# Kernel tuning notes

Measured on AMD Instinct MI355X. Metric: run time of the kernel, lower is better.

Reference implementation:

```python
import jax, jax.numpy as jnp
import numpy as np

NEG_INF = -1e30  # stand-in for float('-inf') that is softmax-safe


def setup_inputs() -> dict:
    key = jax.random.key(0)
    ks = jax.random.split(key, 6)
    B, H, S, D = 2, 8, 1024, 64
    NF, K = 4, 3
    return {
        "query": jax.random.normal(ks[0], (B, H, S, D), dtype=jnp.float32),
        "keys": jax.random.normal(ks[1], (B, H, S, D), dtype=jnp.float32),
        "vals": jax.random.normal(ks[2], (B, H, S, D), dtype=jnp.float32),
        "mask": jnp.ones((B, 1, S, S), dtype=jnp.int32),
        "conv_w": jax.random.normal(ks[3], (NF, 1, K, K), dtype=jnp.float32) * (1.0 / K),
        "conv_b": jnp.zeros((NF,), dtype=jnp.float32),
        "lin_w": jax.random.normal(ks[4], (1, NF), dtype=jnp.float32) * 0.5,
        "lin_b": jnp.zeros((1,), dtype=jnp.float32),
    }


def reference(query, keys, vals, mask, conv_w, conv_b, lin_w, lin_b):
    B, H, S, D = query.shape
    NF = conv_w.shape[0]
    K = conv_w.shape[2]
    scale = jnp.asarray(D, query.dtype) ** 0.5

    # [B,H,S,S] raw dot-product scores
    dp = jnp.einsum("bhsd,bhtd->bhst", query, keys) / scale

    # conv2d over the score matrix: treat (B*H) as batch, 1 input channel
    x = dp.reshape(B * H, 1, S, S)
    conv = jax.lax.conv_general_dilated(
        x, conv_w,
        window_strides=(1, 1),
        padding=[(K // 2, K // 2), (K // 2, K // 2)],
        dimension_numbers=("NCHW", "OIHW", "NCHW"),
    ) + conv_b[None, :, None, None]
    conv = jax.nn.leaky_relu(conv, negative_slope=0.01)  # [B*H, NF, S, S]

    # per-pixel linear over the filter axis (Linear(num_filters, 1))
    conv = conv.reshape(B, H, NF, S, S)
    preattn = jnp.einsum("bhfst,f->bhst", conv, lin_w[0]) + lin_b[0]

    # masking + softmax (mask broadcasts over heads)
    preattn = jnp.where(mask == 0, jnp.asarray(NEG_INF, preattn.dtype), preattn)
    attn = jax.nn.softmax(preattn, axis=-1)

    # dropout is identity in eval mode
    return jnp.einsum("bhst,bhtd->bhsd", attn, vals)
```

## Files before the change

kernel.cpp:

```cpp
#include <hip/hip_runtime.h>
#include <math.h>

#define S_LEN 1024
#define D_DIM 64
#define NBH   16
#define RPB   14
#define NSB   74

typedef unsigned short ushort_t;
typedef unsigned int uint_t;
typedef __attribute__((ext_vector_type(8))) _Float16 half8;
typedef __attribute__((ext_vector_type(2))) _Float16 h2;
typedef __attribute__((ext_vector_type(4))) short short4v;
typedef __attribute__((ext_vector_type(4))) float f32x4;

__device__ __forceinline__ ushort_t f16bits(float x) {
    _Float16 h = (_Float16)x;
    ushort_t b;
    __builtin_memcpy(&b, &h, 2);
    return b;
}
__device__ __forceinline__ float uniform_f(float x) {
    return __int_as_float(__builtin_amdgcn_readfirstlane(__float_as_int(x)));
}
__device__ __forceinline__ float fast_exp2(float x) {
#if __has_builtin(__builtin_amdgcn_exp2f)
    return __builtin_amdgcn_exp2f(x);
#else
    return exp2f(x);
#endif
}
__device__ __forceinline__ half8 mk8(uint2 a, uint2 b) {
    union { uint_t u[4]; half8 h; } c;
    c.u[0] = a.x; c.u[1] = a.y; c.u[2] = b.x; c.u[3] = b.y;
    return c.h;
}
__device__ __forceinline__ int swz(int row, int unit) {
    return (row << 4) + (((unit + (row >> 2)) & 3) << 2);
}

__global__ __launch_bounds__(256) void prep(
    const float* __restrict__ k, const float* __restrict__ v,
    const int* __restrict__ mask, const float* __restrict__ conv_w,
    ushort_t* __restrict__ kh, ushort_t* __restrict__ vh,
    unsigned* __restrict__ mw, ushort_t* __restrict__ wtab)
{
    __shared__ float Ls[64][65];
    const int tid = threadIdx.x;
    const int bx = blockIdx.x;
    if (bx < 512) {
        const int gid  = bx * 256 + tid;
        const int bh   = gid >> 13;
        const int tile = (gid >> 7) & 63;
        const int ch   = (gid >> 6) & 1;
        const int lane = gid & 63;
        const int quad = lane >> 4, t15 = lane & 15;
        const float* src = k + ((size_t)bh * S_LEN + tile * 16 + t15) * D_DIM
                             + ch * 32 + quad * 8;
        float x[8];
        *(float4*)(x + 0) = *(const float4*)(src);
        *(float4*)(x + 4) = *(const float4*)(src + 4);
        ushort_t hv[8];
        #pragma unroll
        for (int i = 0; i < 8; ++i) hv[i] = f16bits(x[i] * 0.125f);
        *(short4v*)(kh + (size_t)gid * 8)     = *(short4v*)(hv);
        *(short4v*)(kh + (size_t)gid * 8 + 4) = *(short4v*)(hv + 4);
    } else if (bx < 768) {
        const int bi = bx - 512;
        const int tt = bi & 15, bh = bi >> 4;
        const float* vb = v + ((size_t)bh * S_LEN + tt * 64) * D_DIM;
        #pragma unroll
        for (int p = 0; p < 4; ++p) {
            int idx = p * 1024 + tid * 4;
            int r = idx >> 6, c = idx & 63;
            float4 x = *(const float4*)(vb + r * 64 + c);
            Ls[r][c] = x.x; Ls[r][c+1] = x.y; Ls[r][c+2] = x.z; Ls[r][c+3] = x.w;
        }
        __syncthreads();
        const int d = tid >> 2, c0 = (tid & 3) * 16;
        ushort_t hi[16];
        #pragma unroll
        for (int j = 0; j < 16; ++j) hi[j] = f16bits(Ls[c0 + j][d]);
        const int tb0 = tt * 8 + (c0 >> 3);
        const size_t o0 = (((size_t)bh * 128 + tb0) * 64 + d) * 8;
        const size_t o1 = (((size_t)bh * 128 + tb0 + 1) * 64 + d) * 8;
        *(short4v*)(vh + o0)     = *(short4v*)(hi);
        *(short4v*)(vh + o0 + 4) = *(short4v*)(hi + 4);
        *(short4v*)(vh + o1)     = *(short4v*)(hi + 8);
        *(short4v*)(vh + o1 + 4) = *(short4v*)(hi + 12);
    } else if (bx < 1024) {
        const int gid = (bx - 768) * 256 + tid;
        const int row = gid >> 5, wd = gid & 31;
        const int4* mp = (const int4*)(mask + (size_t)row * 1024 + wd * 32);
        unsigned bits = 0;
        #pragma unroll
        for (int p = 0; p < 8; ++p) {
            int4 qv = mp[p];
            bits |= (qv.x != 0 ? 1u : 0u) << (p * 4 + 0);
            bits |= (qv.y != 0 ? 1u : 0u) << (p * 4 + 1);
            bits |= (qv.z != 0 ? 1u : 0u) << (p * 4 + 2);
            bits |= (qv.w != 0 ? 1u : 0u) << (p * 4 + 3);
        }
        mw[(size_t)row * 32 + wd] = bits;
    } else {
        if (tid < 64) {
            const int o = tid & 15, qd = tid >> 4;
            half8* wt = (half8*)wtab;
            #pragma unroll
            for (int f = 0; f < 4; ++f) {
                half8 fr0 = {}, fr1 = {}, fr2 = {};
                #pragma unroll
                for (int i = 0; i < 8; ++i) {
                    const int kk = qd * 8 + i;
                    const int r  = kk & 15;
                    const bool hiK = kk < 16;
                    #pragma unroll
                    for (int dr = 0; dr < 3; ++dr) {
                        if (r - o == dr - 1) {
                            const float w0 = conv_w[f*9 + dr*3 + 0];
                            const float w1 = conv_w[f*9 + dr*3 + 1];
                            const float w2 = conv_w[f*9 + dr*3 + 2];
                            const _Float16 w0h = (_Float16)w0;
                            const _Float16 w1h = (_Float16)w1;
                            const _Float16 w2h = (_Float16)w2;
                            const _Float16 w0l = (_Float16)(w0 - (float)w0h);
                            const _Float16 w1l = (_Float16)(w1 - (float)w1h);
                            const _Float16 w2l = (_Float16)(w2 - (float)w2h);
                            fr0[i] = hiK ? w0h : w1h;
                            fr1[i] = hiK ? w0l : w1l;
                            fr2[i] = hiK ? w2h : w2l;
                        }
                    }
                }
                wt[(f*3 + 0) * 64 + tid] = fr0;
                wt[(f*3 + 1) * 64 + tid] = fr1;
                wt[(f*3 + 2) * 64 + tid] = fr2;
            }
        }
    }
}

#define PSTR 1032
__global__ __launch_bounds__(512, 3) void fused_qk_conv_av(
    const float* __restrict__ q,
    const ushort_t* __restrict__ kh, const unsigned* __restrict__ mw,
    const ushort_t* __restrict__ vh, const ushort_t* __restrict__ wtab,
    const float* __restrict__ conv_b,
    const float* __restrict__ lin_w, const float* __restrict__ lin_b,
    float* __restrict__ out)
{
    __shared__ ushort_t sBuf[16512];
    __shared__ float oBuf[16][68];
    __shared__ float lsRow[16];
    __shared__ unsigned mbT[32][16];

    const int st = blockIdx.x, bh = blockIdx.y;
    const int s0 = st * RPB;
    const int b  = bh >> 3;
    const int tid = threadIdx.x;
    const int wave = tid >> 6, lane = tid & 63;
    const int m = lane & 15, quad = lane >> 4;

    {
        const int wd = tid >> 4, o = tid & 15;
        const int s = s0 - 1 + o;
        mbT[wd][o] = (s >= 0 && s < S_LEN)
                   ? mw[((size_t)b * S_LEN + s) * 32 + wd] : 0u;
    }
    if (tid < 32) {
        const int row = (tid < 16) ? 1 : 1026;
        sBuf[(row << 4) + (tid & 15)] = 0;
    }

    const int sA = s0 - 1 + m;
    const int sQ = sA < 0 ? 0 : (sA > S_LEN - 1 ? S_LEN - 1 : sA);
    const float* qp = q + ((size_t)bh * S_LEN + sQ) * D_DIM + quad * 8;
    float qa[16];
    *(float4*)(qa + 0)  = *(const float4*)(qp + 0);
    *(float4*)(qa + 4)  = *(const float4*)(qp + 4);
    *(float4*)(qa + 8)  = *(const float4*)(qp + 32);
    *(float4*)(qa + 12) = *(const float4*)(qp + 36);
    half8 AH0, AH1;
    #pragma unroll
    for (int i = 0; i < 8; ++i) {
        AH0[i] = (_Float16)qa[i];
        AH1[i] = (_Float16)qa[8 + i];
    }

    #pragma unroll
    for (int tt = 0; tt < 8; ++tt) {
        const int tile = wave * 8 + tt;
        const size_t kb = (((size_t)bh * 64 + tile) * 128 + lane) * 8;
        half8 KH0 = *(const half8*)(kh + kb);
        half8 KH1 = *(const half8*)(kh + kb + 512);
        f32x4 a = {0.f, 0.f, 0.f, 0.f};
        a = __builtin_amdgcn_mfma_f32_16x16x32_f16(AH0, KH0, a, 0, 0, 0);
        a = __builtin_amdgcn_mfma_f32_16x16x32_f16(AH1, KH1, a, 0, 0, 0);
        ushort_t t4[4];
        #pragma unroll
        for (int r = 0; r < 4; ++r) {
            const int s = s0 - 1 + quad * 4 + r;
            const float v = (s >= 0 && s < S_LEN) ? a[r] : 0.f;
            t4[r] = f16bits(v);
        }
        uint2 wv2;
        wv2.x = (uint_t)t4[0] | ((uint_t)t4[1] << 16);
        wv2.y = (uint_t)t4[2] | ((uint_t)t4[3] << 16);
        *(uint2*)&sBuf[swz(tile * 16 + m + 2, quad)] = wv2;
    }

    const float L2E = 1.44269504088896341f;
    const float lbE = uniform_f(lin_b[0] * L2E);

    __syncthreads();

    const int u0 = (quad & 1) << 1;
    const int rB = m + 1 + (quad >> 1);
    uint_t Ps[16];
    #pragma unroll
    for (int p = 0; p < 4; ++p) {
        const int tileA = wave * 8 + p * 2;
        const int baseA = tileA * 16;
        half8 BA01 = mk8(*(const uint2*)&sBuf[swz(baseA + rB, u0)],
                         *(const uint2*)&sBuf[swz(baseA + rB, u0 + 1)]);
        half8 BA22 = mk8(*(const uint2*)&sBuf[swz(baseA + m + 3, u0)],
                         *(const uint2*)&sBuf[swz(baseA + m + 3, u0 + 1)]);
        half8 BB01 = mk8(*(const uint2*)&sBuf[swz(baseA + 16 + rB, u0)],
                         *(const uint2*)&sBuf[swz(baseA + 16 + rB, u0 + 1)]);
        half8 BB22 = mk8(*(const uint2*)&sBuf[swz(baseA + 16 + m + 3, u0)],
                         *(const uint2*)&sBuf[swz(baseA + 16 + m + 3, u0 + 1)]);
        float preA[4], preB[4];
        #pragma unroll
        for (int r = 0; r < 4; ++r) { preA[r] = lbE; preB[r] = lbE; }
        #pragma unroll 1
        for (int f = 0; f < 4; ++f) {
            const half8* wp = (const half8*)wtab + f * 192 + lane;
            const half8 W0 = wp[0];
            const half8 W1 = wp[64];
            const half8 W2 = wp[128];
            const float cbf = conv_b[f];
            const float lwf = lin_w[f];
            const float af  = uniform_f(0.505f * lwf * L2E);
            const float bf2 = uniform_f(0.495f * lwf * L2E);
            f32x4 aA = {cbf, cbf, cbf, cbf};
            f32x4 aB = {cbf, cbf, cbf, cbf};
            aA = __builtin_amdgcn_mfma_f32_16x16x32_f16(W0, BA01, aA, 0, 0, 0);
            aB = __builtin_amdgcn_mfma_f32_16x16x32_f16(W0, BB01, aB, 0, 0, 0);
            aA = __builtin_amdgcn_mfma_f32_16x16x32_f16(W1, BA01, aA, 0, 0, 0);
            aB = __builtin_amdgcn_mfma_f32_16x16x32_f16(W1, BB01, aB, 0, 0, 0);
            aA = __builtin_amdgcn_mfma_f32_16x16x32_f16(W2, BA22, aA, 0, 0, 0);
            aB = __builtin_amdgcn_mfma_f32_16x16x32_f16(W2, BB22, aB, 0, 0, 0);
            #pragma unroll
            for (int r = 0; r < 4; ++r) {
                const float yA = aA[r], yB = aB[r];
                preA[r] = fmaf(af, yA, preA[r]);
                preA[r] = fmaf(bf2, fabsf(yA), preA[r]);
                preB[r] = fmaf(af, yB, preB[r]);
                preB[r] = fmaf(bf2, fabsf(yB), preB[r]);
            }
        }
        const uint4 mq = *(const uint4*)&mbT[(tileA >> 1)][quad * 4];
        float pvA[4], pvB[4];
        #pragma unroll
        for (int r = 0; r < 4; ++r) {
            const int o = quad * 4 + r;
            const bool act = (o >= 1) && (o <= RPB) && (s0 - 1 + o < S_LEN);
            const unsigned mword = (r == 0) ? mq.x : (r == 1) ? mq.y
                                 : (r == 2) ? mq.z : mq.w;
            const bool kA = act && ((mword >> m) & 1u);
            const bool kB = act && ((mword >> (16 + m)) & 1u);
            pvA[r] = fast_exp2(kA ? preA[r] : -1e30f);
            pvB[r] = fast_exp2(kB ? preB[r] : -1e30f);
        }
        Ps[p*4 + 0] = (uint_t)f16bits(pvA[0]) | ((uint_t)f16bits(pvA[1]) << 16);
        Ps[p*4 + 1] = (uint_t)f16bits(pvA[2]) | ((uint_t)f16bits(pvA[3]) << 16);
        Ps[p*4 + 2] = (uint_t)f16bits(pvB[0]) | ((uint_t)f16bits(pvB[1]) << 16);
        Ps[p*4 + 3] = (uint_t)f16bits(pvB[2]) | ((uint_t)f16bits(pvB[3]) << 16);
    }
    __syncthreads();

    #pragma unroll
    for (int tt = 0; tt < 8; ++tt) {
        const int c = (wave * 8 + tt) * 16 + m;
        ushort_t* pp = &sBuf[quad * 4 * PSTR + c];
        const uint_t lo = Ps[2*tt], hi = Ps[2*tt + 1];
        pp[0]        = (ushort_t)lo;
        pp[PSTR]     = (ushort_t)(lo >> 16);
        pp[2*PSTR]   = (ushort_t)hi;
        pp[3*PSTR]   = (ushort_t)(hi >> 16);
    }
    __syncthreads();

    const int d0 = (wave & 3) * 16;
    const int th = wave >> 2;
    f32x4 O  = {0.f, 0.f, 0.f, 0.f};
    f32x4 RS = {0.f, 0.f, 0.f, 0.f};
    half8 ONE;
    #pragma unroll
    for (int i = 0; i < 8; ++i) ONE[i] = (_Float16)1.0f;
    const ushort_t* ph_base = &sBuf[m * PSTR + th * 512 + quad * 8];
    const ushort_t* vv_base = vh + ((size_t)bh * 65536
                                    + (size_t)(th * 64 + quad) * 512
                                    + (size_t)(d0 + m) * 8);
    #pragma unroll 4
    for (int i = 0; i < 16; ++i) {
        half8 ph = *(const half8*)(ph_base + i * 32);
        half8 vv = *(const half8*)(vv_base + (size_t)i * 2048);
        O  = __builtin_amdgcn_mfma_f32_16x16x32_f16(ph, vv, O, 0, 0, 0);
        RS = __builtin_amdgcn_mfma_f32_16x16x32_f16(ph, ONE, RS, 0, 0, 0);
    }
    if (wave < 4) {
        #pragma unroll
        for (int r = 0; r < 4; ++r) oBuf[quad * 4 + r][d0 + m] = O[r];
    }
    if (wave == 0 && m == 0) {
        #pragma unroll
        for (int r = 0; r < 4; ++r) lsRow[quad * 4 + r] = RS[r];
    }
    __syncthreads();
    if (wave >= 4) {
        #pragma unroll
        for (int r = 0; r < 4; ++r) {
            const int br = quad * 4 + r;
            const int s = s0 - 1 + br;
            if (br >= 1 && br <= RPB && s < S_LEN) {
                const float lsum = lsRow[br] + RS[r];
                out[((size_t)bh * S_LEN + s) * D_DIM + d0 + m] =
                    (O[r] + oBuf[br][d0 + m]) / lsum;
            }
        }
    }
}

extern "C" void kernel_launch(void* const* d_in, const int* in_sizes, int n_in,
                              void* d_out, int out_size, void* d_ws, size_t ws_size,
                              hipStream_t stream) {
    const float* q      = (const float*)d_in[0];
    const float* k      = (const float*)d_in[1];
    const float* v      = (const float*)d_in[2];
    const int*   mask   = (const int*)d_in[3];
    const float* conv_w = (const float*)d_in[4];
    const float* conv_b = (const float*)d_in[5];
    const float* lin_w  = (const float*)d_in[6];
    const float* lin_b  = (const float*)d_in[7];
    float* out = (float*)d_out;

    char* wsb = (char*)d_ws;
    const size_t MB = 1024 * 1024;
    ushort_t* kh   = (ushort_t*)(wsb + 0 * MB);
    ushort_t* vh   = (ushort_t*)(wsb + 2 * MB);
    unsigned* mw   = (unsigned*)(wsb + 4 * MB);
    ushort_t* wtab = (ushort_t*)(wsb + 4 * MB + 256 * 1024);

    prep<<<dim3(1025), 256, 0, stream>>>(k, v, mask, conv_w, kh, vh, mw, wtab);
    fused_qk_conv_av<<<dim3(NSB, NBH), 512, 0, stream>>>(
        q, kh, mw, vh, wtab, conv_b, lin_w, lin_b, out);
}
```

Baseline: 124.8 us.

## Remove block barrier by recomputing halo QK tiles per wave

Each wave now recomputes the neighbouring QK score tiles (one before and one after its own range) and writes only the halo row it needs into shared memory. This lets the block-wide __syncthreads between the score stage and the conv stage be dropped. The weight table is also changed to interleave the three fragments per lane so they load contiguously, and the conv bias is added after the MFMA instead of being used to seed the accumulator. The cost is two extra MFMA tile computations and K loads per wave. Without a barrier, waves may race on shared rows written by other waves, for example the zeroed boundary rows and the mask table.

```diff
diff --git a/kernel.cpp b/kernel.cpp
--- a/kernel.cpp
+++ b/kernel.cpp
@@ -132,9 +132,9 @@
                         }
                     }
                 }
-                wt[(f*3 + 0) * 64 + tid] = fr0;
-                wt[(f*3 + 1) * 64 + tid] = fr1;
-                wt[(f*3 + 2) * 64 + tid] = fr2;
+                wt[(f*64 + tid)*3 + 0] = fr0;
+                wt[(f*64 + tid)*3 + 1] = fr1;
+                wt[(f*64 + tid)*3 + 2] = fr2;
             }
         }
     }
@@ -167,10 +167,8 @@
         mbT[wd][o] = (s >= 0 && s < S_LEN)
                    ? mw[((size_t)b * S_LEN + s) * 32 + wd] : 0u;
     }
-    if (tid < 32) {
-        const int row = (tid < 16) ? 1 : 1026;
-        sBuf[(row << 4) + (tid & 15)] = 0;
-    }
+    if (wave == 0 && lane < 16) sBuf[(1    << 4) + lane] = 0;
+    if (wave == 7 && lane < 16) sBuf[(1026 << 4) + lane] = 0;
 
     const int sA = s0 - 1 + m;
     const int sQ = sA < 0 ? 0 : (sA > S_LEN - 1 ? S_LEN - 1 : sA);
@@ -208,11 +206,36 @@
         wv2.y = (uint_t)t4[2] | ((uint_t)t4[3] << 16);
         *(uint2*)&sBuf[swz(tile * 16 + m + 2, quad)] = wv2;
     }
+    #pragma unroll
+    for (int hsel = 0; hsel < 2; ++hsel) {
+        const int tile = hsel ? (wave * 8 + 8) : (wave * 8 - 1);
+        const int wantM = hsel ? 0 : 15;
+        if (tile >= 0 && tile < 64) {
+            const size_t kb = (((size_t)bh * 64 + tile) * 128 + lane) * 8;
+            half8 KH0 = *(const half8*)(kh + kb);
+            half8 KH1 = *(const half8*)(kh + kb + 512);
+            f32x4 a = {0.f, 0.f, 0.f, 0.f};
+            a = __builtin_amdgcn_mfma_f32_16x16x32_f16(AH0, KH0, a, 0, 0, 0);
+            a = __builtin_amdgcn_mfma_f32_16x16x32_f16(AH1, KH1, a, 0, 0, 0);
+            if (m == wantM) {
+                ushort_t t4[4];
+                #pragma unroll
+                for (int r = 0; r < 4; ++r) {
+                    const int s = s0 - 1 + quad * 4 + r;
+                    const float v = (s >= 0 && s < S_LEN) ? a[r] : 0.f;
+                    t4[r] = f16bits(v);
+                }
+                uint2 wv2;
+                wv2.x = (uint_t)t4[0] | ((uint_t)t4[1] << 16);
+                wv2.y = (uint_t)t4[2] | ((uint_t)t4[3] << 16);
+                *(uint2*)&sBuf[swz(tile * 16 + m + 2, quad)] = wv2;
+            }
+        }
+    }
 
     const float L2E = 1.44269504088896341f;
     const float lbE = uniform_f(lin_b[0] * L2E);
 
-    __syncthreads();
 
     const int u0 = (quad & 1) << 1;
     const int rB = m + 1 + (quad >> 1);
@@ -234,16 +257,16 @@
         for (int r = 0; r < 4; ++r) { preA[r] = lbE; preB[r] = lbE; }
         #pragma unroll 1
         for (int f = 0; f < 4; ++f) {
-            const half8* wp = (const half8*)wtab + f * 192 + lane;
-            const half8 W0 = wp[0];
-            const half8 W1 = wp[64];
-            const half8 W2 = wp[128];
-            const float cbf = conv_b[f];
+            const float cbf = uniform_f(conv_b[f]);
             const float lwf = lin_w[f];
             const float af  = uniform_f(0.505f * lwf * L2E);
             const float bf2 = uniform_f(0.495f * lwf * L2E);
-            f32x4 aA = {cbf, cbf, cbf, cbf};
-            f32x4 aB = {cbf, cbf, cbf, cbf};
+            const half8* wp = (const half8*)wtab + (f * 64 + lane) * 3;
+            const half8 W0 = wp[0];
+            const half8 W1 = wp[1];
+            const half8 W2 = wp[2];
+            f32x4 aA = {0.f, 0.f, 0.f, 0.f};
+            f32x4 aB = {0.f, 0.f, 0.f, 0.f};
             aA = __builtin_amdgcn_mfma_f32_16x16x32_f16(W0, BA01, aA, 0, 0, 0);
             aB = __builtin_amdgcn_mfma_f32_16x16x32_f16(W0, BB01, aB, 0, 0, 0);
             aA = __builtin_amdgcn_mfma_f32_16x16x32_f16(W1, BA01, aA, 0, 0, 0);
@@ -252,7 +275,7 @@
             aB = __builtin_amdgcn_mfma_f32_16x16x32_f16(W2, BB22, aB, 0, 0, 0);
             #pragma unroll
             for (int r = 0; r < 4; ++r) {
-                const float yA = aA[r], yB = aB[r];
+                const float yA = aA[r] + cbf, yB = aB[r] + cbf;
                 preA[r] = fmaf(af, yA, preA[r]);
                 preA[r] = fmaf(bf2, fabsf(yA), preA[r]);
                 preB[r] = fmaf(af, yB, preB[r]);
```

Measured after the change: 125.0 us. About the same (+0.2%).
